# Optimization experiments

Measured on AMD Instinct MI355X. Metric: run time of the kernel, lower is better.

The kernel has to match this reference:

```python
import jax, jax.numpy as jnp
import numpy as np

NEG_SLOPE = 0.2
EPS = 1e-16  # PyG softmax denominator epsilon


def _gatv2_layer(x, src, dst, n_nodes, W_l, W_r, att, bias):
    """Single-head GATv2Conv (PyG defaults, self loops already in src/dst).
    x: [N, F_in]; src/dst: [E]; W_l/W_r: [F_in, F_out]; att: [F_out]; bias: [F_out].
    """
    x_l = x @ W_l                       # source transform [N, F_out]
    x_r = x @ W_r                       # target transform [N, F_out]
    # per-edge attention logit: a^T LeakyReLU(x_l[j] + x_r[i])
    e = jax.nn.leaky_relu(x_l[src] + x_r[dst], NEG_SLOPE) @ att  # [E]
    # softmax over incoming edges of each destination node
    e_max = jax.ops.segment_max(e, dst, num_segments=n_nodes)    # [N]
    ex = jnp.exp(e - e_max[dst])                                  # [E]
    denom = jax.ops.segment_sum(ex, dst, num_segments=n_nodes)   # [N]
    alpha = ex / (denom[dst] + EPS)                               # [E]
    out = jax.ops.segment_sum(alpha[:, None] * x_l[src], dst, num_segments=n_nodes)
    return out + bias


def setup_inputs() -> dict:
    key = jax.random.key(0)
    N, E = 50000, 800000
    IN, HID, OUT = 128, 64, 64
    ks = jax.random.split(key, 12)
    x = jax.random.normal(ks[0], (N, IN), dtype=jnp.float32)
    edge_index = jax.random.randint(ks[1], (2, E), 0, N, dtype=jnp.int64)
    s1 = float(1.0 / np.sqrt(IN))
    s2 = float(1.0 / np.sqrt(HID))
    return {
        "x": x,
        "edge_index": edge_index,
        "W1_l": jax.random.uniform(ks[2], (IN, HID), jnp.float32, -s1, s1),
        "W1_r": jax.random.uniform(ks[3], (IN, HID), jnp.float32, -s1, s1),
        "att1": jax.random.uniform(ks[4], (HID,), jnp.float32, -s2, s2),
        "b1": jnp.zeros((HID,), jnp.float32),
        "W2_l": jax.random.uniform(ks[5], (HID, OUT), jnp.float32, -s2, s2),
        "W2_r": jax.random.uniform(ks[6], (HID, OUT), jnp.float32, -s2, s2),
        "att2": jax.random.uniform(ks[7], (OUT,), jnp.float32, -s2, s2),
        "b2": jnp.zeros((OUT,), jnp.float32),
    }


def reference(x, edge_index, W1_l, W1_r, att1, b1, W2_l, W2_r, att2, b2):
    n = x.shape[0]
    loop = jnp.arange(n, dtype=edge_index.dtype)
    src = jnp.concatenate([edge_index[0], loop])  # add self loops (PyG default)
    dst = jnp.concatenate([edge_index[1], loop])
    h = _gatv2_layer(x, src, dst, n, W1_l, W1_r, att1, b1)
    h = jax.nn.relu(h)
    out = _gatv2_layer(h, src, dst, n, W2_l, W2_r, att2, b2)
    return out
```

## Files before the change

### kernel.cpp

```cpp
#include <hip/hip_runtime.h>
#include <math.h>

#define NEG_SLOPE 0.2f
#define EPSV 1e-16f
#define NEG_HUGE -1e30f
#define CAP 64

typedef short short8 __attribute__((ext_vector_type(8)));
typedef float f32x4 __attribute__((ext_vector_type(4)));
typedef unsigned short u16;

__global__ __launch_bounds__(256) void k_wpack(
        const float* __restrict__ W1l, const float* __restrict__ W1r,
        const float* __restrict__ W2l, const float* __restrict__ W2r,
        u16* __restrict__ w1hi, u16* __restrict__ w1lo,
        u16* __restrict__ w2hi, u16* __restrict__ w2lo,
        int* __restrict__ cnt, int N) {
    const int idx = blockIdx.x * 256 + threadIdx.x;
    const int G = gridDim.x * 256;
    for (int i = idx; i < N; i += G) cnt[i] = 0;
    const int T1 = 128 * 128, T2 = 64 * 128;
    if (idx >= T1 + T2) return;
    u16 *dhi, *dlo; const float *Wl, *Wr; int li;
    if (idx < T1) { dhi = w1hi; dlo = w1lo; Wl = W1l; Wr = W1r; li = idx; }
    else          { dhi = w2hi; dlo = w2lo; Wl = W2l; Wr = W2r; li = idx - T1; }
    const int j = li & 7, l = (li >> 3) & 63, t = (li >> 9) & 7, c = li >> 12;
    const int k = c * 32 + (l >> 4) * 8 + j;
    const int n = t * 16 + (l & 15);
    const float v = (n < 64) ? Wl[k * 64 + n] : Wr[k * 64 + (n - 64)];
    const unsigned u = __float_as_uint(v);
    dhi[li] = (u16)(u >> 16);
    const float hif = __uint_as_float(u & 0xffff0000u);
    dlo[li] = (u16)(__float_as_uint(v - hif) >> 16);
}

template <int K>
__device__ __forceinline__ void gemm_mfma_tile(const float* __restrict__ X,
                                               const u16* __restrict__ whi,
                                               const u16* __restrict__ wlo,
                                               float* __restrict__ xl,
                                               float* __restrict__ xr,
                                               int N, int tile) {
    const int lane = threadIdx.x & 63;
    const int w = threadIdx.x >> 6;
    const int rowbase = tile * 64 + w * 16;
    const int m = lane & 15, q = lane >> 4;
    int ar = rowbase + m; if (ar > N - 1) ar = N - 1;
    const float* arow = X + (size_t)ar * K + q * 8;
    f32x4 acc[8];
#pragma unroll
    for (int t = 0; t < 8; ++t) acc[t] = (f32x4){0.f, 0.f, 0.f, 0.f};
#pragma unroll
    for (int c = 0; c < K / 32; ++c) {
        const float4 f0 = *(const float4*)(arow + c * 32);
        const float4 f1 = *(const float4*)(arow + c * 32 + 4);
        const float fs[8] = {f0.x, f0.y, f0.z, f0.w, f1.x, f1.y, f1.z, f1.w};
        short8 ahi, alo;
#pragma unroll
        for (int j = 0; j < 8; ++j) {
            const unsigned u = __float_as_uint(fs[j]);
            ahi[j] = (short)(u >> 16);
            const float hif = __uint_as_float(u & 0xffff0000u);
            alo[j] = (short)(__float_as_uint(fs[j] - hif) >> 16);
        }
        const u16* bp = whi + ((size_t)(c * 8) * 64 + lane) * 8;
        const u16* bq = wlo + ((size_t)(c * 8) * 64 + lane) * 8;
#pragma unroll
        for (int t = 0; t < 8; ++t) {
            const short8 bhi = *(const short8*)(bp + t * 64 * 8);
            const short8 blo = *(const short8*)(bq + t * 64 * 8);
            acc[t] = __builtin_amdgcn_mfma_f32_16x16x32_bf16(ahi, bhi, acc[t], 0, 0, 0);
            acc[t] = __builtin_amdgcn_mfma_f32_16x16x32_bf16(ahi, blo, acc[t], 0, 0, 0);
            acc[t] = __builtin_amdgcn_mfma_f32_16x16x32_bf16(alo, bhi, acc[t], 0, 0, 0);
        }
    }
#pragma unroll
    for (int t = 0; t < 8; ++t) {
        const int col = t * 16 + m;
        float* dstp = (col < 64) ? (xl + col) : (xr + col - 64);
#pragma unroll
        for (int r = 0; r < 4; ++r) {
            const int row = rowbase + q * 4 + r;
            if (row < N) dstp[(size_t)row * 64] = acc[t][r];
        }
    }
}

template <int K>
__global__ __launch_bounds__(256) void k_hist_gemm(const int* __restrict__ ei, int E, int ET,
                                                   int* __restrict__ cnt,
                                                   u16* __restrict__ csrc, int GH,
                                                   const float* __restrict__ X,
                                                   const u16* __restrict__ whi,
                                                   const u16* __restrict__ wlo,
                                                   float* __restrict__ xl,
                                                   float* __restrict__ xr, int N) {
    if ((int)blockIdx.x < GH) {
        const int gt = blockIdx.x * 256 + threadIdx.x;
        const int G = GH * 256;
        for (int e = gt; e < ET; e += G) {
            int src, dst;
            if (e < E) { src = ei[e]; dst = ei[E + e]; }
            else       { src = dst = e - E; }
            const int slot = atomicAdd(&cnt[dst], 1);
            csrc[(size_t)dst * CAP + slot] = (u16)src;
        }
    } else {
        gemm_mfma_tile<K>(X, whi, wlo, xl, xr, N, blockIdx.x - GH);
    }
}

template <int K>
__global__ __launch_bounds__(256) void k_gemm(const float* __restrict__ X,
                                              const u16* __restrict__ whi,
                                              const u16* __restrict__ wlo,
                                              float* __restrict__ xl,
                                              float* __restrict__ xr, int N) {
    gemm_mfma_tile<K>(X, whi, wlo, xl, xr, N, blockIdx.x);
}

__global__ __launch_bounds__(256) void k_attn(const float* __restrict__ xl,
                                              const float* xr,
                                              const float* __restrict__ att,
                                              const int* __restrict__ cnt,
                                              const u16* __restrict__ csrc,
                                              const float* __restrict__ bias,
                                              float* out, int N, int relu) {
    const int lane = threadIdx.x & 63;
    const int g = lane >> 4;
    const int i = lane & 15;
    const int dst = blockIdx.x * 4 + (threadIdx.x >> 6);
    if (dst >= N) return;
    const float4 xrv = *(const float4*)(xr + (size_t)dst * 64 + i * 4);
    const float4 aw  = *(const float4*)(att + i * 4);
    const int deg = cnt[dst];
    const int sidx = (int)csrc[(size_t)dst * CAP + ((lane < deg) ? lane : 0)];
    float l = 0.0f;
    float4 acc = {0.0f, 0.0f, 0.0f, 0.0f};
    for (int t = 0; t < deg; t += 16) {
        const int s0 = t + g, s1 = t + 4 + g, s2 = t + 8 + g, s3 = t + 12 + g;
        const bool v0 = s0 < deg, v1 = s1 < deg, v2 = s2 < deg, v3 = s3 < deg;
        const int src0 = __shfl(sidx, s0, 64);
        const int src1 = __shfl(sidx, s1, 64);
        const int src2 = __shfl(sidx, s2, 64);
        const int src3 = __shfl(sidx, s3, 64);
        const float4 va = *(const float4*)(xl + (size_t)src0 * 64 + i * 4);
        const float4 vb = *(const float4*)(xl + (size_t)src1 * 64 + i * 4);
        const float4 vc = *(const float4*)(xl + (size_t)src2 * 64 + i * 4);
        const float4 vd = *(const float4*)(xl + (size_t)src3 * 64 + i * 4);
        float t0, p0, p1, p2, p3;
        t0 = va.x + xrv.x; t0 = fmaxf(t0, NEG_SLOPE * t0); p0 = aw.x * t0;
        t0 = va.y + xrv.y; t0 = fmaxf(t0, NEG_SLOPE * t0); p0 = fmaf(aw.y, t0, p0);
        t0 = va.z + xrv.z; t0 = fmaxf(t0, NEG_SLOPE * t0); p0 = fmaf(aw.z, t0, p0);
        t0 = va.w + xrv.w; t0 = fmaxf(t0, NEG_SLOPE * t0); p0 = fmaf(aw.w, t0, p0);
        t0 = vb.x + xrv.x; t0 = fmaxf(t0, NEG_SLOPE * t0); p1 = aw.x * t0;
        t0 = vb.y + xrv.y; t0 = fmaxf(t0, NEG_SLOPE * t0); p1 = fmaf(aw.y, t0, p1);
        t0 = vb.z + xrv.z; t0 = fmaxf(t0, NEG_SLOPE * t0); p1 = fmaf(aw.z, t0, p1);
        t0 = vb.w + xrv.w; t0 = fmaxf(t0, NEG_SLOPE * t0); p1 = fmaf(aw.w, t0, p1);
        t0 = vc.x + xrv.x; t0 = fmaxf(t0, NEG_SLOPE * t0); p2 = aw.x * t0;
        t0 = vc.y + xrv.y; t0 = fmaxf(t0, NEG_SLOPE * t0); p2 = fmaf(aw.y, t0, p2);
        t0 = vc.z + xrv.z; t0 = fmaxf(t0, NEG_SLOPE * t0); p2 = fmaf(aw.z, t0, p2);
        t0 = vc.w + xrv.w; t0 = fmaxf(t0, NEG_SLOPE * t0); p2 = fmaf(aw.w, t0, p2);
        t0 = vd.x + xrv.x; t0 = fmaxf(t0, NEG_SLOPE * t0); p3 = aw.x * t0;
        t0 = vd.y + xrv.y; t0 = fmaxf(t0, NEG_SLOPE * t0); p3 = fmaf(aw.y, t0, p3);
        t0 = vd.z + xrv.z; t0 = fmaxf(t0, NEG_SLOPE * t0); p3 = fmaf(aw.z, t0, p3);
        t0 = vd.w + xrv.w; t0 = fmaxf(t0, NEG_SLOPE * t0); p3 = fmaf(aw.w, t0, p3);
        p0 += __shfl_xor(p0, 1, 64); p1 += __shfl_xor(p1, 1, 64);
        p2 += __shfl_xor(p2, 1, 64); p3 += __shfl_xor(p3, 1, 64);
        p0 += __shfl_xor(p0, 2, 64); p1 += __shfl_xor(p1, 2, 64);
        p2 += __shfl_xor(p2, 2, 64); p3 += __shfl_xor(p3, 2, 64);
        p0 += __shfl_xor(p0, 4, 64); p1 += __shfl_xor(p1, 4, 64);
        p2 += __shfl_xor(p2, 4, 64); p3 += __shfl_xor(p3, 4, 64);
        p0 += __shfl_xor(p0, 8, 64); p1 += __shfl_xor(p1, 8, 64);
        p2 += __shfl_xor(p2, 8, 64); p3 += __shfl_xor(p3, 8, 64);
        const float d0 = __expf(v0 ? p0 : NEG_HUGE);
        const float d1 = __expf(v1 ? p1 : NEG_HUGE);
        const float d2 = __expf(v2 ? p2 : NEG_HUGE);
        const float d3 = __expf(v3 ? p3 : NEG_HUGE);
        l += (d0 + d1) + (d2 + d3);
        acc.x = fmaf(d0, va.x, fmaf(d1, vb.x, fmaf(d2, vc.x, fmaf(d3, vd.x, acc.x))));
        acc.y = fmaf(d0, va.y, fmaf(d1, vb.y, fmaf(d2, vc.y, fmaf(d3, vd.y, acc.y))));
        acc.z = fmaf(d0, va.z, fmaf(d1, vb.z, fmaf(d2, vc.z, fmaf(d3, vd.z, acc.z))));
        acc.w = fmaf(d0, va.w, fmaf(d1, vb.w, fmaf(d2, vc.w, fmaf(d3, vd.w, acc.w))));
    }
#pragma unroll
    for (int o = 16; o <= 32; o <<= 1) {
        l     += __shfl_xor(l, o, 64);
        acc.x += __shfl_xor(acc.x, o, 64);
        acc.y += __shfl_xor(acc.y, o, 64);
        acc.z += __shfl_xor(acc.z, o, 64);
        acc.w += __shfl_xor(acc.w, o, 64);
    }
    if (g == 0) {
        const float4 bv = *(const float4*)(bias + i * 4);
        const float inv = 1.0f / (l + EPSV);
        float4 r;
        r.x = fmaf(acc.x, inv, bv.x);
        r.y = fmaf(acc.y, inv, bv.y);
        r.z = fmaf(acc.z, inv, bv.z);
        r.w = fmaf(acc.w, inv, bv.w);
        if (relu) {
            r.x = fmaxf(r.x, 0.0f); r.y = fmaxf(r.y, 0.0f);
            r.z = fmaxf(r.z, 0.0f); r.w = fmaxf(r.w, 0.0f);
        }
        *(float4*)(out + (size_t)dst * 64 + i * 4) = r;
    }
}


extern "C" void kernel_launch(void* const* d_in, const int* in_sizes, int n_in,
                              void* d_out, int out_size, void* d_ws, size_t ws_size,
                              hipStream_t stream) {
    const float* x    = (const float*)d_in[0];
    const int*   ei   = (const int*)d_in[1];
    const float* W1l  = (const float*)d_in[2];
    const float* W1r  = (const float*)d_in[3];
    const float* att1 = (const float*)d_in[4];
    const float* b1   = (const float*)d_in[5];
    const float* W2l  = (const float*)d_in[6];
    const float* W2r  = (const float*)d_in[7];
    const float* att2 = (const float*)d_in[8];
    const float* b2   = (const float*)d_in[9];

    const int N  = in_sizes[0] / 128;
    const int E  = in_sizes[1] / 2;
    const int ET = E + N;
    const int GH = 512;

    int* wsi   = (int*)d_ws;
    int* cnt   = wsi;
    u16* csrc  = (u16*)(cnt + N);
    u16* w1hi  = csrc + (size_t)N * CAP;
    u16* w1lo  = w1hi + 16384;
    u16* w2hi  = w1lo + 16384;
    u16* w2lo  = w2hi + 8192;
    float* buf1 = (float*)(w2lo + 8192);
    float* buf2 = buf1 + (size_t)N * 64;
    float* fout = (float*)d_out;

    const dim3 b256(256);
    const int gGemm = (N + 63) / 64;
    const int gAttn = (N + 3) / 4;

    k_wpack<<<(128 * 128 + 64 * 128 + 255) / 256, b256, 0, stream>>>(
        W1l, W1r, W2l, W2r, w1hi, w1lo, w2hi, w2lo, cnt, N);

    k_hist_gemm<128><<<GH + gGemm, b256, 0, stream>>>(ei, E, ET, cnt, csrc, GH,
                                                      x, w1hi, w1lo, fout, buf1, N);
    k_attn<<<gAttn, b256, 0, stream>>>(fout, buf1, att1, cnt, csrc, b1, buf2, N, 1);

    k_gemm<64><<<gGemm, b256, 0, stream>>>(buf2, w2hi, w2lo, buf1, fout, N);
    k_attn<<<gAttn, b256, 0, stream>>>(buf1, fout, att2, cnt, csrc, b2, fout, N, 0);
}
```

Measured before the change: 226.5 us.

## Fuse layer-1 attention with layer-2 GEMM through shared memory

Layer-1 attention now runs inside a tile kernel that aggregates 64 destination nodes into LDS, then applies the layer-2 hi/lo bf16 MFMA projection directly from LDS. This drops one kernel launch and the global write and re-read of the hidden activations. In exchange each wave processes 16 destination nodes serially and the grid shrinks by a factor of 16 blocks-wise, which lowers memory-level parallelism in the gather-heavy attention phase. A third workspace buffer is added.

```diff
diff --git a/kernel.cpp b/kernel.cpp
--- a/kernel.cpp
+++ b/kernel.cpp
@@ -34,6 +34,16 @@
     dlo[li] = (u16)(__float_as_uint(v - hif) >> 16);
 }
 
+__device__ __forceinline__ void split8(const float* fs, short8& ahi, short8& alo) {
+#pragma unroll
+    for (int j = 0; j < 8; ++j) {
+        const unsigned u = __float_as_uint(fs[j]);
+        ahi[j] = (short)(u >> 16);
+        const float hif = __uint_as_float(u & 0xffff0000u);
+        alo[j] = (short)(__float_as_uint(fs[j] - hif) >> 16);
+    }
+}
+
 template <int K>
 __device__ __forceinline__ void gemm_mfma_tile(const float* __restrict__ X,
                                                const u16* __restrict__ whi,
@@ -56,13 +66,7 @@
         const float4 f1 = *(const float4*)(arow + c * 32 + 4);
         const float fs[8] = {f0.x, f0.y, f0.z, f0.w, f1.x, f1.y, f1.z, f1.w};
         short8 ahi, alo;
-#pragma unroll
-        for (int j = 0; j < 8; ++j) {
-            const unsigned u = __float_as_uint(fs[j]);
-            ahi[j] = (short)(u >> 16);
-            const float hif = __uint_as_float(u & 0xffff0000u);
-            alo[j] = (short)(__float_as_uint(fs[j] - hif) >> 16);
-        }
+        split8(fs, ahi, alo);
         const u16* bp = whi + ((size_t)(c * 8) * 64 + lane) * 8;
         const u16* bq = wlo + ((size_t)(c * 8) * 64 + lane) * 8;
 #pragma unroll
@@ -110,29 +114,12 @@
     }
 }
 
-template <int K>
-__global__ __launch_bounds__(256) void k_gemm(const float* __restrict__ X,
-                                              const u16* __restrict__ whi,
-                                              const u16* __restrict__ wlo,
-                                              float* __restrict__ xl,
-                                              float* __restrict__ xr, int N) {
-    gemm_mfma_tile<K>(X, whi, wlo, xl, xr, N, blockIdx.x);
-}
-
-__global__ __launch_bounds__(256) void k_attn(const float* __restrict__ xl,
-                                              const float* xr,
-                                              const float* __restrict__ att,
-                                              const int* __restrict__ cnt,
-                                              const u16* __restrict__ csrc,
-                                              const float* __restrict__ bias,
-                                              float* out, int N, int relu) {
-    const int lane = threadIdx.x & 63;
-    const int g = lane >> 4;
-    const int i = lane & 15;
-    const int dst = blockIdx.x * 4 + (threadIdx.x >> 6);
-    if (dst >= N) return;
-    const float4 xrv = *(const float4*)(xr + (size_t)dst * 64 + i * 4);
-    const float4 aw  = *(const float4*)(att + i * 4);
+__device__ __forceinline__ float4 attn_body(const float* __restrict__ xl,
+                                            const float4 xrv, const float4 aw,
+                                            const int* __restrict__ cnt,
+                                            const u16* __restrict__ csrc,
+                                            const float4 bv, int relu, int dst,
+                                            int lane, int g, int i) {
     const int deg = cnt[dst];
     const int sidx = (int)csrc[(size_t)dst * CAP + ((lane < deg) ? lane : 0)];
     float l = 0.0f;
@@ -191,20 +178,96 @@
         acc.z += __shfl_xor(acc.z, o, 64);
         acc.w += __shfl_xor(acc.w, o, 64);
     }
-    if (g == 0) {
-        const float4 bv = *(const float4*)(bias + i * 4);
-        const float inv = 1.0f / (l + EPSV);
-        float4 r;
-        r.x = fmaf(acc.x, inv, bv.x);
-        r.y = fmaf(acc.y, inv, bv.y);
-        r.z = fmaf(acc.z, inv, bv.z);
-        r.w = fmaf(acc.w, inv, bv.w);
-        if (relu) {
-            r.x = fmaxf(r.x, 0.0f); r.y = fmaxf(r.y, 0.0f);
-            r.z = fmaxf(r.z, 0.0f); r.w = fmaxf(r.w, 0.0f);
-        }
-        *(float4*)(out + (size_t)dst * 64 + i * 4) = r;
-    }
+    const float inv = 1.0f / (l + EPSV);
+    float4 r;
+    r.x = fmaf(acc.x, inv, bv.x);
+    r.y = fmaf(acc.y, inv, bv.y);
+    r.z = fmaf(acc.z, inv, bv.z);
+    r.w = fmaf(acc.w, inv, bv.w);
+    if (relu) {
+        r.x = fmaxf(r.x, 0.0f); r.y = fmaxf(r.y, 0.0f);
+        r.z = fmaxf(r.z, 0.0f); r.w = fmaxf(r.w, 0.0f);
+    }
+    return r;
+}
+
+__global__ __launch_bounds__(256) void k_attn_gemm(
+        const float* __restrict__ xl, const float* __restrict__ xr,
+        const float* __restrict__ att, const int* __restrict__ cnt,
+        const u16* __restrict__ csrc, const float* __restrict__ bias,
+        const u16* __restrict__ whi, const u16* __restrict__ wlo,
+        float* __restrict__ oxl, float* __restrict__ oxr, int N) {
+    __shared__ float hs[64][68];
+    const int tile = blockIdx.x;
+    const int lane = threadIdx.x & 63;
+    const int w = threadIdx.x >> 6;
+    const int g = lane >> 4, i = lane & 15;
+    const int base = tile * 64;
+    const float4 aw = *(const float4*)(att + i * 4);
+    const float4 bv = *(const float4*)(bias + i * 4);
+    for (int j = 0; j < 16; ++j) {
+        const int dloc = w * 16 + j;
+        const int dst = base + dloc;
+        if (dst < N) {
+            const float4 xrv = *(const float4*)(xr + (size_t)dst * 64 + i * 4);
+            const float4 r = attn_body(xl, xrv, aw, cnt, csrc, bv, 1, dst, lane, g, i);
+            if (g == 0) *(float4*)&hs[dloc][i * 4] = r;
+        } else if (g == 0) {
+            *(float4*)&hs[dloc][i * 4] = (float4){0.f, 0.f, 0.f, 0.f};
+        }
+    }
+    __syncthreads();
+    const int m = i, q = g;
+    f32x4 acc[8];
+#pragma unroll
+    for (int t = 0; t < 8; ++t) acc[t] = (f32x4){0.f, 0.f, 0.f, 0.f};
+#pragma unroll
+    for (int c = 0; c < 2; ++c) {
+        const float* ap = &hs[w * 16 + m][c * 32 + q * 8];
+        const float4 f0 = *(const float4*)ap;
+        const float4 f1 = *(const float4*)(ap + 4);
+        const float fs[8] = {f0.x, f0.y, f0.z, f0.w, f1.x, f1.y, f1.z, f1.w};
+        short8 ahi, alo;
+        split8(fs, ahi, alo);
+        const u16* bp = whi + ((size_t)(c * 8) * 64 + lane) * 8;
+        const u16* bq = wlo + ((size_t)(c * 8) * 64 + lane) * 8;
+#pragma unroll
+        for (int t = 0; t < 8; ++t) {
+            const short8 bhi = *(const short8*)(bp + t * 64 * 8);
+            const short8 blo = *(const short8*)(bq + t * 64 * 8);
+            acc[t] = __builtin_amdgcn_mfma_f32_16x16x32_bf16(ahi, bhi, acc[t], 0, 0, 0);
+            acc[t] = __builtin_amdgcn_mfma_f32_16x16x32_bf16(ahi, blo, acc[t], 0, 0, 0);
+            acc[t] = __builtin_amdgcn_mfma_f32_16x16x32_bf16(alo, bhi, acc[t], 0, 0, 0);
+        }
+    }
+#pragma unroll
+    for (int t = 0; t < 8; ++t) {
+        const int col = t * 16 + m;
+        float* dstp = (col < 64) ? (oxl + col) : (oxr + col - 64);
+#pragma unroll
+        for (int r = 0; r < 4; ++r) {
+            const int row = base + w * 16 + q * 4 + r;
+            if (row < N) dstp[(size_t)row * 64] = acc[t][r];
+        }
+    }
+}
+
+__global__ __launch_bounds__(256) void k_attn(const float* __restrict__ xl,
+                                              const float* __restrict__ xr,
+                                              const float* __restrict__ att,
+                                              const int* __restrict__ cnt,
+                                              const u16* __restrict__ csrc,
+                                              const float* __restrict__ bias,
+                                              float* __restrict__ out, int N, int relu) {
+    const int lane = threadIdx.x & 63;
+    const int g = lane >> 4, i = lane & 15;
+    const int dst = blockIdx.x * 4 + (threadIdx.x >> 6);
+    if (dst >= N) return;
+    const float4 xrv = *(const float4*)(xr + (size_t)dst * 64 + i * 4);
+    const float4 aw  = *(const float4*)(att + i * 4);
+    const float4 bv  = *(const float4*)(bias + i * 4);
+    const float4 r = attn_body(xl, xrv, aw, cnt, csrc, bv, relu, dst, lane, g, i);
+    if (g == 0) *(float4*)(out + (size_t)dst * 64 + i * 4) = r;
 }
 
 
@@ -236,6 +299,7 @@
     u16* w2lo  = w2hi + 8192;
     float* buf1 = (float*)(w2lo + 8192);
     float* buf2 = buf1 + (size_t)N * 64;
+    float* buf3 = buf2 + (size_t)N * 64;
     float* fout = (float*)d_out;
 
     const dim3 b256(256);
@@ -247,8 +311,9 @@
 
     k_hist_gemm<128><<<GH + gGemm, b256, 0, stream>>>(ei, E, ET, cnt, csrc, GH,
                                                       x, w1hi, w1lo, fout, buf1, N);
-    k_attn<<<gAttn, b256, 0, stream>>>(fout, buf1, att1, cnt, csrc, b1, buf2, N, 1);
-
-    k_gemm<64><<<gGemm, b256, 0, stream>>>(buf2, w2hi, w2lo, buf1, fout, N);
-    k_attn<<<gAttn, b256, 0, stream>>>(buf1, fout, att2, cnt, csrc, b2, fout, N, 0);
-}
+
+    k_attn_gemm<<<gGemm, b256, 0, stream>>>(fout, buf1, att1, cnt, csrc, b1,
+                                            w2hi, w2lo, buf2, buf3, N);
+
+    k_attn<<<gAttn, b256, 0, stream>>>(buf2, buf3, att2, cnt, csrc, b2, fout, N, 0);
+}
```

New measurement: 263.9 us. 16.5% more time.
